# Performance work log

Measured on AMD Instinct MI355X. Metric: run time of the kernel, lower is better.

## Reference

```python
import jax, jax.numpy as jnp
import numpy as np

WINDOW = 7
HEADS = 8
DIM_HEAD = 32
NUM_MEM = 4
EPS = 1e-5


def _rel_pos_indices(window):
    pos = np.arange(window)
    gi, gj = np.meshgrid(pos, pos, indexing='ij')
    grid = np.stack([gi.ravel(), gj.ravel()], axis=-1)          # [w*w, 2]
    rel = grid[:, None, :] - grid[None, :, :] + (window - 1)    # [n, n, 2]
    return jnp.asarray(rel[..., 0] * (2 * window - 1) + rel[..., 1])  # [n, n]


def setup_inputs() -> dict:
    key = jax.random.key(0)
    ks = jax.random.split(key, 5)
    dim = 256
    return {
        'x': jax.random.normal(ks[0], (16, 16, 16, 7, 7, dim), jnp.float32),
        'gamma': jnp.ones((dim,), jnp.float32),
        'w_qkv': jax.random.normal(ks[1], (dim, 3 * dim), jnp.float32) * 0.02,
        'mem_kv': jax.random.normal(ks[2], (2, HEADS, NUM_MEM, DIM_HEAD), jnp.float32),
        'rel_bias_table': jax.random.normal(ks[3], ((2 * WINDOW - 1) ** 2, HEADS), jnp.float32) * 0.02,
        'w_out': jax.random.normal(ks[4], (dim, dim), jnp.float32) * 0.02,
    }


def reference(x, gamma, w_qkv, mem_kv, rel_bias_table, w_out):
    b, H, W, w1, w2, d = x.shape
    n = w1 * w2
    B = b * H * W
    scale = DIM_HEAD ** -0.5

    # LayerNorm (beta fixed at 0)
    mu = x.mean(-1, keepdims=True)
    var = ((x - mu) ** 2).mean(-1, keepdims=True)
    xn = (x - mu) * jax.lax.rsqrt(var + EPS) * gamma

    xw = xn.reshape(B, n, d)
    qkv = xw @ w_qkv                                  # [B, n, 3d]
    q, k, v = jnp.split(qkv, 3, axis=-1)
    to_heads = lambda t: t.reshape(B, n, HEADS, DIM_HEAD).transpose(0, 2, 1, 3)  # bhnd
    q = to_heads(q) * scale
    k = to_heads(k)
    v = to_heads(v)

    # memory kv, broadcast over batch-of-windows
    mk = jnp.broadcast_to(mem_kv[0][None], (B, HEADS, NUM_MEM, DIM_HEAD))
    mv = jnp.broadcast_to(mem_kv[1][None], (B, HEADS, NUM_MEM, DIM_HEAD))
    k = jnp.concatenate([mk, k], axis=2)              # [B, h, num_mem + n, dh]
    v = jnp.concatenate([mv, v], axis=2)

    sim = jnp.einsum('bhid,bhjd->bhij', q, k)         # [B, h, n, num_mem + n]

    idx = _rel_pos_indices(WINDOW)                    # [n, n] int
    bias = rel_bias_table[idx]                        # [n, n, h]
    bias = jnp.pad(bias, ((0, 0), (NUM_MEM, 0), (0, 0)))  # pad keys at front
    sim = sim + bias.transpose(2, 0, 1)[None]         # [1, h, n, num_mem + n]

    attn = jax.nn.softmax(sim, axis=-1)
    out = jnp.einsum('bhij,bhjd->bhid', attn, v)      # [B, h, n, dh]
    out = out.transpose(0, 2, 1, 3).reshape(B, w1, w2, d)
    out = out @ w_out
    return out.reshape(b, H, W, w1, w2, d)
```

## Files before the change

### kernel.cpp

```cpp
#include <hip/hip_runtime.h>
#include <hip/hip_bf16.h>

typedef __attribute__((ext_vector_type(8))) short bf16x8;
typedef __attribute__((ext_vector_type(4))) float f32x4;

#define NWIN   4096
#define NTOK   49
#define DMODEL 256
#define NHEAD  8
#define DHEAD  32
#define NKEY   53
#define LDX    264
#define LDQK   40
#define LDP    72
#define LDVT   72
#define QK_SHORTS 2560
#define VT_SHORTS 2304
#define PERHEAD   7424
#define LDS_SHORTS (PERHEAD * 8)
#define LDS_BYTES  (LDS_SHORTS * 2)

__device__ __forceinline__ short f2bf(float f) {
  unsigned u = __float_as_uint(f);
  unsigned r = (u + 0x7fffu + ((u >> 16) & 1u)) >> 16;
  return (short)r;
}

__device__ __forceinline__ f32x4 mfma16(bf16x8 a, bf16x8 b, f32x4 c) {
  return __builtin_amdgcn_mfma_f32_16x16x32_bf16(a, b, c, 0, 0, 0);
}

__global__ void k_convert(const float* __restrict__ wqkv, const float* __restrict__ wout,
                          short* __restrict__ wqT, short* __restrict__ woT) {
  int idx = blockIdx.x * 256 + threadIdx.x;
  if (idx < 768 * 256) {
    int n = idx >> 8, k = idx & 255;
    wqT[idx] = f2bf(wqkv[k * 768 + n]);
  }
  if (idx < 256 * 256) {
    int n = idx >> 8, k = idx & 255;
    woT[idx] = f2bf(wout[k * 256 + n]);
  }
}

__global__ __launch_bounds__(512, 2) void k_attn(
    const float* __restrict__ x, const float* __restrict__ gamma,
    const short* __restrict__ wqT, const float* __restrict__ memkv,
    const float* __restrict__ btab, short* __restrict__ aout) {
  extern __shared__ short lds[];
  const int tid = threadIdx.x;
  const int wv = tid >> 6;
  const int lane = tid & 63;
  const int lhi = lane >> 4, llo = lane & 15;
  const int win = blockIdx.x;

  {
    int* w = (int*)lds;
    for (int j = tid; j < 64 * LDX / 2; j += 512) w[j] = 0;
  }
  __syncthreads();

  const float* xwin = x + (size_t)win * (NTOK * DMODEL);
  const float4 g4 = ((const float4*)gamma)[lane];
  for (int row = wv; row < NTOK; row += 8) {
    float4 v = ((const float4*)(xwin + row * DMODEL))[lane];
    float s = v.x + v.y + v.z + v.w;
#pragma unroll
    for (int m = 1; m < 64; m <<= 1) s += __shfl_xor(s, m);
    float mu = s * (1.0f / 256.0f);
    float dx = v.x - mu, dy = v.y - mu, dz = v.z - mu, dw = v.w - mu;
    float s2 = dx * dx + dy * dy + dz * dz + dw * dw;
#pragma unroll
    for (int m = 1; m < 64; m <<= 1) s2 += __shfl_xor(s2, m);
    float rs = rsqrtf(s2 * (1.0f / 256.0f) + 1e-5f);
    short4 o;
    o.x = f2bf(dx * rs * g4.x); o.y = f2bf(dy * rs * g4.y);
    o.z = f2bf(dz * rs * g4.z); o.w = f2bf(dw * rs * g4.w);
    *(short4*)&lds[row * LDX + lane * 4] = o;
  }
  __syncthreads();

  const int h = wv;
  f32x4 acc[4][6] = {};
  {
    const int nr = h * 32 + llo;
    const int nrow[6] = {nr, nr + 16, nr + 256, nr + 272, nr + 512, nr + 528};
    for (int ks = 0; ks < 8; ++ks) {
      bf16x8 a[4];
#pragma unroll
      for (int mt = 0; mt < 4; ++mt)
        a[mt] = *(const bf16x8*)&lds[(mt * 16 + llo) * LDX + ks * 32 + lhi * 8];
#pragma unroll
      for (int nt = 0; nt < 6; ++nt) {
        bf16x8 b = *(const bf16x8*)&wqT[nrow[nt] * 256 + ks * 32 + lhi * 8];
#pragma unroll
        for (int mt = 0; mt < 4; ++mt) acc[mt][nt] = mfma16(a[mt], b, acc[mt][nt]);
      }
    }
  }
  __syncthreads();

  short* qh = lds + wv * PERHEAD;
  short* kh = qh + QK_SHORTS;
  short* vth = kh + QK_SHORTS;
  short* Ph = qh;

  {
    int* w = (int*)qh;
    for (int i = lane; i < PERHEAD / 2; i += 64) w[i] = 0;
  }

  const float qscale = 0.17677669529663687f;
#pragma unroll
  for (int mt = 0; mt < 4; ++mt)
#pragma unroll
    for (int r = 0; r < 4; ++r) {
      int row = mt * 16 + lhi * 4 + r;
      if (row < NTOK) {
        qh[row * LDQK + llo]            = f2bf(acc[mt][0][r] * qscale);
        qh[row * LDQK + 16 + llo]       = f2bf(acc[mt][1][r] * qscale);
        kh[(row + 4) * LDQK + llo]      = f2bf(acc[mt][2][r]);
        kh[(row + 4) * LDQK + 16 + llo] = f2bf(acc[mt][3][r]);
        vth[llo * LDVT + row + 4]        = f2bf(acc[mt][4][r]);
        vth[(llo + 16) * LDVT + row + 4] = f2bf(acc[mt][5][r]);
      }
    }
#pragma unroll
  for (int i = 0; i < 2; ++i) {
    int e = lane + i * 64;
    int m = e >> 5, d = e & 31;
    kh[m * LDQK + d]  = f2bf(memkv[(h * 4 + m) * 32 + d]);
    vth[d * LDVT + m] = f2bf(memkv[1024 + (h * 4 + m) * 32 + d]);
  }

  f32x4 sim[4][4] = {};
  {
    bf16x8 qa[4], kb[4];
#pragma unroll
    for (int mt = 0; mt < 4; ++mt)
      qa[mt] = *(const bf16x8*)&qh[(mt * 16 + llo) * LDQK + lhi * 8];
#pragma unroll
    for (int nt = 0; nt < 4; ++nt)
      kb[nt] = *(const bf16x8*)&kh[(nt * 16 + llo) * LDQK + lhi * 8];
#pragma unroll
    for (int nt = 0; nt < 4; ++nt)
#pragma unroll
      for (int mt = 0; mt < 4; ++mt) sim[mt][nt] = mfma16(qa[mt], kb[nt], sim[mt][nt]);
  }

#pragma unroll
  for (int mt = 0; mt < 4; ++mt)
#pragma unroll
    for (int r = 0; r < 4; ++r) {
      const int qt = mt * 16 + lhi * 4 + r;
      const bool qv = qt < NTOK;
      const int qa_ = qt / 7, qb_ = qt % 7;
      float vals[4];
#pragma unroll
      for (int nt = 0; nt < 4; ++nt) {
        int col = nt * 16 + llo;
        float sv = sim[mt][nt][r];
        if (col >= NKEY) sv = -1e30f;
        else if (qv && col >= 4) {
          int t = col - 4;
          int r0 = qa_ - t / 7 + 6, r1 = qb_ - t % 7 + 6;
          sv += btab[(r0 * 13 + r1) * NHEAD + h];
        }
        vals[nt] = sv;
      }
      float mx = fmaxf(fmaxf(vals[0], vals[1]), fmaxf(vals[2], vals[3]));
#pragma unroll
      for (int m = 1; m < 16; m <<= 1) mx = fmaxf(mx, __shfl_xor(mx, m));
      float p[4], sum = 0.f;
#pragma unroll
      for (int nt = 0; nt < 4; ++nt) { p[nt] = __expf(vals[nt] - mx); sum += p[nt]; }
#pragma unroll
      for (int m = 1; m < 16; m <<= 1) sum += __shfl_xor(sum, m);
      float inv = 1.0f / sum;
#pragma unroll
      for (int nt = 0; nt < 4; ++nt)
        Ph[qt * LDP + nt * 16 + llo] = f2bf(p[nt] * inv);
    }

  f32x4 oacc[4][2] = {};
#pragma unroll
  for (int ks = 0; ks < 2; ++ks) {
    bf16x8 pa[4];
#pragma unroll
    for (int mt = 0; mt < 4; ++mt)
      pa[mt] = *(const bf16x8*)&Ph[(mt * 16 + llo) * LDP + ks * 32 + lhi * 8];
#pragma unroll
    for (int nt = 0; nt < 2; ++nt) {
      bf16x8 vb = *(const bf16x8*)&vth[(nt * 16 + llo) * LDVT + ks * 32 + lhi * 8];
#pragma unroll
      for (int mt = 0; mt < 4; ++mt) oacc[mt][nt] = mfma16(pa[mt], vb, oacc[mt][nt]);
    }
  }

  short* ao = aout + (size_t)win * NTOK * DMODEL;
#pragma unroll
  for (int mt = 0; mt < 4; ++mt)
#pragma unroll
    for (int r = 0; r < 4; ++r) {
      int row = mt * 16 + lhi * 4 + r;
      if (row < NTOK) {
#pragma unroll
        for (int nt = 0; nt < 2; ++nt)
          ao[row * DMODEL + h * DHEAD + nt * 16 + llo] = f2bf(oacc[mt][nt][r]);
      }
    }
}

__global__ __launch_bounds__(256, 2) void k_out(
    const short* __restrict__ aout, const short* __restrict__ woT,
    float* __restrict__ out) {
  __shared__ short At[64 * LDX];
  const int tid = threadIdx.x;
  const int wv = tid >> 6, lane = tid & 63;
  const int lhi = lane >> 4, llo = lane & 15;
  const size_t m0 = (size_t)blockIdx.x * 64;
#pragma unroll
  for (int i = 0; i < 8; ++i) {
    int c = tid + i * 256;
    int row = c >> 5, cc = c & 31;
    *(int4*)&At[row * LDX + cc * 8] = *(const int4*)&aout[(m0 + row) * DMODEL + cc * 8];
  }
  __syncthreads();
  f32x4 acc[4][4] = {};
  for (int ks = 0; ks < 8; ++ks) {
    bf16x8 a[4], b[4];
#pragma unroll
    for (int mt = 0; mt < 4; ++mt)
      a[mt] = *(const bf16x8*)&At[(mt * 16 + llo) * LDX + ks * 32 + lhi * 8];
#pragma unroll
    for (int nt = 0; nt < 4; ++nt)
      b[nt] = *(const bf16x8*)&woT[(wv * 64 + nt * 16 + llo) * 256 + ks * 32 + lhi * 8];
#pragma unroll
    for (int nt = 0; nt < 4; ++nt)
#pragma unroll
      for (int mt = 0; mt < 4; ++mt) acc[mt][nt] = mfma16(a[mt], b[nt], acc[mt][nt]);
  }
#pragma unroll
  for (int mt = 0; mt < 4; ++mt)
#pragma unroll
    for (int nt = 0; nt < 4; ++nt)
#pragma unroll
      for (int r = 0; r < 4; ++r)
        out[(m0 + mt * 16 + lhi * 4 + r) * DMODEL + wv * 64 + nt * 16 + llo] = acc[mt][nt][r];
}

extern "C" void kernel_launch(void* const* d_in, const int* in_sizes, int n_in,
                              void* d_out, int out_size, void* d_ws, size_t ws_size,
                              hipStream_t stream) {
  const float* x     = (const float*)d_in[0];
  const float* gamma = (const float*)d_in[1];
  const float* wqkv  = (const float*)d_in[2];
  const float* memkv = (const float*)d_in[3];
  const float* btab  = (const float*)d_in[4];
  const float* wout  = (const float*)d_in[5];
  float* out = (float*)d_out;

  short* wqT  = (short*)d_ws;
  short* woT  = wqT + 768 * 256;
  short* aout = woT + 256 * 256;

  k_convert<<<768, 256, 0, stream>>>(wqkv, wout, wqT, woT);
  k_attn<<<NWIN, 512, LDS_BYTES, stream>>>(x, gamma, wqT, memkv, btab, aout);
  k_out<<<200704 / 64, 256, 0, stream>>>(aout, woT, out);
}
```

Baseline: 858.9 us.

## Split fused LN/QKV/attention kernel into separate QKV and per-head attention kernels

The single large-LDS attention kernel is split in two. k_lnqkv does LayerNorm and the QKV projection, then writes per-head Q, K and transposed V to global memory. k_attn2 runs one wave per (window, head) and computes softmax attention. A prep kernel also precomputes a dense per-head relative-position bias matrix with the padding mask baked in, plus bf16 memory keys, so the softmax loop drops its index arithmetic. The aim is much lower LDS use per block and higher occupancy, at the cost of hundreds of MB of extra global writes and reads for the Q, K and V intermediates.

```diff
diff --git a/kernel.cpp b/kernel.cpp
--- a/kernel.cpp
+++ b/kernel.cpp
@@ -1,24 +1,11 @@
 #include <hip/hip_runtime.h>
-#include <hip/hip_bf16.h>
 
 typedef __attribute__((ext_vector_type(8))) short bf16x8;
 typedef __attribute__((ext_vector_type(4))) float f32x4;
 
-#define NWIN   4096
-#define NTOK   49
-#define DMODEL 256
-#define NHEAD  8
-#define DHEAD  32
-#define NKEY   53
-#define LDX    264
-#define LDQK   40
-#define LDP    72
-#define LDVT   72
-#define QK_SHORTS 2560
-#define VT_SHORTS 2304
-#define PERHEAD   7424
-#define LDS_SHORTS (PERHEAD * 8)
-#define LDS_BYTES  (LDS_SHORTS * 2)
+#define NWIN 4096
+#define NTOK 49
+#define NHEAD 8
 
 __device__ __forceinline__ short f2bf(float f) {
   unsigned u = __float_as_uint(f);
@@ -30,40 +17,45 @@
   return __builtin_amdgcn_mfma_f32_16x16x32_bf16(a, b, c, 0, 0, 0);
 }
 
-__global__ void k_convert(const float* __restrict__ wqkv, const float* __restrict__ wout,
-                          short* __restrict__ wqT, short* __restrict__ woT) {
+__global__ void k_prep(const float* __restrict__ wqkv, const float* __restrict__ wout,
+                       const float* __restrict__ memkv, const float* __restrict__ btab,
+                       short* __restrict__ wqT, short* __restrict__ woT,
+                       short* __restrict__ memB, float* __restrict__ biasF) {
   int idx = blockIdx.x * 256 + threadIdx.x;
-  if (idx < 768 * 256) {
-    int n = idx >> 8, k = idx & 255;
-    wqT[idx] = f2bf(wqkv[k * 768 + n]);
-  }
-  if (idx < 256 * 256) {
-    int n = idx >> 8, k = idx & 255;
-    woT[idx] = f2bf(wout[k * 256 + n]);
-  }
-}
-
-__global__ __launch_bounds__(512, 2) void k_attn(
+  if (idx < 768 * 256) { int n = idx >> 8, k = idx & 255; wqT[idx] = f2bf(wqkv[k * 768 + n]); }
+  if (idx < 256 * 256) { int n = idx >> 8, k = idx & 255; woT[idx] = f2bf(wout[k * 256 + n]); }
+  if (idx < 2048) memB[idx] = f2bf(memkv[idx]);
+  if (idx < 32768) {
+    int h = idx >> 12, qt = (idx >> 6) & 63, col = idx & 63;
+    float b;
+    if (col >= 53) b = -1e30f;
+    else if (col < 4 || qt >= 49) b = 0.f;
+    else {
+      int t = col - 4;
+      int r0 = qt / 7 - t / 7 + 6, r1 = qt % 7 - t % 7 + 6;
+      b = btab[(r0 * 13 + r1) * NHEAD + h];
+    }
+    biasF[idx] = b;
+  }
+}
+
+__global__ __launch_bounds__(512, 4) void k_lnqkv(
     const float* __restrict__ x, const float* __restrict__ gamma,
     const short* __restrict__ wqT, const float* __restrict__ memkv,
-    const float* __restrict__ btab, short* __restrict__ aout) {
-  extern __shared__ short lds[];
+    short* __restrict__ qg, short* __restrict__ kg, short* __restrict__ vtg) {
+  __shared__ short lds[18432];
   const int tid = threadIdx.x;
-  const int wv = tid >> 6;
-  const int lane = tid & 63;
+  const int wv = tid >> 6, lane = tid & 63;
   const int lhi = lane >> 4, llo = lane & 15;
-  const int win = blockIdx.x;
-
-  {
-    int* w = (int*)lds;
-    for (int j = tid; j < 64 * LDX / 2; j += 512) w[j] = 0;
-  }
-  __syncthreads();
-
-  const float* xwin = x + (size_t)win * (NTOK * DMODEL);
+  const int win = blockIdx.x, h = wv;
+
+  for (int j = tid; j < 8448; j += 512) ((int*)lds)[j] = 0;
+  __syncthreads();
+
+  const float* xwin = x + (size_t)win * (NTOK * 256);
   const float4 g4 = ((const float4*)gamma)[lane];
   for (int row = wv; row < NTOK; row += 8) {
-    float4 v = ((const float4*)(xwin + row * DMODEL))[lane];
+    float4 v = ((const float4*)(xwin + row * 256))[lane];
     float s = v.x + v.y + v.z + v.w;
 #pragma unroll
     for (int m = 1; m < 64; m <<= 1) s += __shfl_xor(s, m);
@@ -76,98 +68,128 @@
     short4 o;
     o.x = f2bf(dx * rs * g4.x); o.y = f2bf(dy * rs * g4.y);
     o.z = f2bf(dz * rs * g4.z); o.w = f2bf(dw * rs * g4.w);
-    *(short4*)&lds[row * LDX + lane * 4] = o;
-  }
-  __syncthreads();
-
-  const int h = wv;
-  f32x4 acc[4][6] = {};
+    *(short4*)&lds[row * 264 + lane * 4] = o;
+  }
+  __syncthreads();
+
+  const int nr = h * 32 + llo;
+  f32x4 a1[4][4] = {};
+  for (int ks = 0; ks < 8; ++ks) {
+    bf16x8 a[4];
+#pragma unroll
+    for (int mt = 0; mt < 4; ++mt)
+      a[mt] = *(const bf16x8*)&lds[(mt * 16 + llo) * 264 + ks * 32 + lhi * 8];
+    const int nrow[4] = {nr, nr + 16, nr + 256, nr + 272};
+#pragma unroll
+    for (int nt = 0; nt < 4; ++nt) {
+      bf16x8 b = *(const bf16x8*)&wqT[nrow[nt] * 256 + ks * 32 + lhi * 8];
+#pragma unroll
+      for (int mt = 0; mt < 4; ++mt) a1[mt][nt] = mfma16(a[mt], b, a1[mt][nt]);
+    }
+  }
   {
-    const int nr = h * 32 + llo;
-    const int nrow[6] = {nr, nr + 16, nr + 256, nr + 272, nr + 512, nr + 528};
-    for (int ks = 0; ks < 8; ++ks) {
-      bf16x8 a[4];
-#pragma unroll
-      for (int mt = 0; mt < 4; ++mt)
-        a[mt] = *(const bf16x8*)&lds[(mt * 16 + llo) * LDX + ks * 32 + lhi * 8];
-#pragma unroll
-      for (int nt = 0; nt < 6; ++nt) {
-        bf16x8 b = *(const bf16x8*)&wqT[nrow[nt] * 256 + ks * 32 + lhi * 8];
-#pragma unroll
-        for (int mt = 0; mt < 4; ++mt) acc[mt][nt] = mfma16(a[mt], b, acc[mt][nt]);
+    const float qscale = 0.17677669529663687f;
+    short* qdst = qg + (size_t)(win * 8 + h) * (NTOK * 32);
+    short* kdst = kg + (size_t)(win * 8 + h) * (NTOK * 32);
+#pragma unroll
+    for (int mt = 0; mt < 4; ++mt)
+#pragma unroll
+      for (int r = 0; r < 4; ++r) {
+        int row = mt * 16 + lhi * 4 + r;
+        if (row < NTOK) {
+          qdst[row * 32 + llo]      = f2bf(a1[mt][0][r] * qscale);
+          qdst[row * 32 + llo + 16] = f2bf(a1[mt][1][r] * qscale);
+          kdst[row * 32 + llo]      = f2bf(a1[mt][2][r]);
+          kdst[row * 32 + llo + 16] = f2bf(a1[mt][3][r]);
+        }
       }
-    }
-  }
-  __syncthreads();
-
-  short* qh = lds + wv * PERHEAD;
-  short* kh = qh + QK_SHORTS;
-  short* vth = kh + QK_SHORTS;
-  short* Ph = qh;
-
-  {
-    int* w = (int*)qh;
-    for (int i = lane; i < PERHEAD / 2; i += 64) w[i] = 0;
-  }
-
-  const float qscale = 0.17677669529663687f;
+  }
+  f32x4 a2[4][2] = {};
+  for (int ks = 0; ks < 8; ++ks) {
+    bf16x8 a[4];
+#pragma unroll
+    for (int mt = 0; mt < 4; ++mt)
+      a[mt] = *(const bf16x8*)&lds[(mt * 16 + llo) * 264 + ks * 32 + lhi * 8];
+    const int nrow[2] = {nr + 512, nr + 528};
+#pragma unroll
+    for (int nt = 0; nt < 2; ++nt) {
+      bf16x8 b = *(const bf16x8*)&wqT[nrow[nt] * 256 + ks * 32 + lhi * 8];
+#pragma unroll
+      for (int mt = 0; mt < 4; ++mt) a2[mt][nt] = mfma16(a[mt], b, a2[mt][nt]);
+    }
+  }
+  __syncthreads();
+  for (int j = tid; j < 9216; j += 512) ((int*)lds)[j] = 0;
+  __syncthreads();
+
+  short* vth = lds + wv * 2304;
 #pragma unroll
   for (int mt = 0; mt < 4; ++mt)
 #pragma unroll
     for (int r = 0; r < 4; ++r) {
       int row = mt * 16 + lhi * 4 + r;
       if (row < NTOK) {
-        qh[row * LDQK + llo]            = f2bf(acc[mt][0][r] * qscale);
-        qh[row * LDQK + 16 + llo]       = f2bf(acc[mt][1][r] * qscale);
-        kh[(row + 4) * LDQK + llo]      = f2bf(acc[mt][2][r]);
-        kh[(row + 4) * LDQK + 16 + llo] = f2bf(acc[mt][3][r]);
-        vth[llo * LDVT + row + 4]        = f2bf(acc[mt][4][r]);
-        vth[(llo + 16) * LDVT + row + 4] = f2bf(acc[mt][5][r]);
+        vth[llo * 72 + row + 4]        = f2bf(a2[mt][0][r]);
+        vth[(llo + 16) * 72 + row + 4] = f2bf(a2[mt][1][r]);
       }
     }
 #pragma unroll
   for (int i = 0; i < 2; ++i) {
-    int e = lane + i * 64;
-    int m = e >> 5, d = e & 31;
-    kh[m * LDQK + d]  = f2bf(memkv[(h * 4 + m) * 32 + d]);
-    vth[d * LDVT + m] = f2bf(memkv[1024 + (h * 4 + m) * 32 + d]);
-  }
+    int e = lane + i * 64, m = e >> 5, d = e & 31;
+    vth[d * 72 + m] = f2bf(memkv[1024 + (h * 4 + m) * 32 + d]);
+  }
+#pragma unroll
+  for (int i = 0; i < 4; ++i) {
+    int c = lane + i * 64, row = c >> 3, co = c & 7;
+    bf16x8 t = *(const bf16x8*)&vth[row * 72 + co * 8];
+    *(bf16x8*)&vtg[((size_t)(win * 8 + h) * 32 + row) * 64 + co * 8] = t;
+  }
+}
+
+__global__ __launch_bounds__(256, 4) void k_attn2(
+    const short* __restrict__ qg, const short* __restrict__ kg,
+    const short* __restrict__ vtg, const short* __restrict__ memB,
+    const float* __restrict__ biasF, short* __restrict__ aout) {
+  __shared__ short P[4][64 * 72];
+  const int tid = threadIdx.x;
+  const int wv = tid >> 6, lane = tid & 63;
+  const int lhi = lane >> 4, llo = lane & 15;
+  const int pid = blockIdx.x * 4 + wv;
+  const int win = pid >> 3, h = pid & 7;
+
+  const short* qp = qg + (size_t)pid * (NTOK * 32);
+  const short* kp = kg + (size_t)pid * (NTOK * 32);
+  const short* vp = vtg + (size_t)pid * (32 * 64);
+
+  bf16x8 qa[4], kb[4];
+#pragma unroll
+  for (int mt = 0; mt < 4; ++mt)
+    qa[mt] = *(const bf16x8*)&qp[(mt * 16 + llo) * 32 + lhi * 8];
+  {
+    const short* p = (llo < 4) ? &memB[(h * 4 + llo) * 32] : &kp[(llo - 4) * 32];
+    kb[0] = *(const bf16x8*)&p[lhi * 8];
+  }
+#pragma unroll
+  for (int nt = 1; nt < 4; ++nt)
+    kb[nt] = *(const bf16x8*)&kp[(nt * 16 + llo - 4) * 32 + lhi * 8];
 
   f32x4 sim[4][4] = {};
-  {
-    bf16x8 qa[4], kb[4];
-#pragma unroll
-    for (int mt = 0; mt < 4; ++mt)
-      qa[mt] = *(const bf16x8*)&qh[(mt * 16 + llo) * LDQK + lhi * 8];
-#pragma unroll
-    for (int nt = 0; nt < 4; ++nt)
-      kb[nt] = *(const bf16x8*)&kh[(nt * 16 + llo) * LDQK + lhi * 8];
-#pragma unroll
-    for (int nt = 0; nt < 4; ++nt)
-#pragma unroll
-      for (int mt = 0; mt < 4; ++mt) sim[mt][nt] = mfma16(qa[mt], kb[nt], sim[mt][nt]);
-  }
-
+#pragma unroll
+  for (int nt = 0; nt < 4; ++nt)
+#pragma unroll
+    for (int mt = 0; mt < 4; ++mt) sim[mt][nt] = mfma16(qa[mt], kb[nt], sim[mt][nt]);
+
+  short* Ph = P[wv];
+  const float* bh = biasF + h * 4096;
 #pragma unroll
   for (int mt = 0; mt < 4; ++mt)
 #pragma unroll
     for (int r = 0; r < 4; ++r) {
       const int qt = mt * 16 + lhi * 4 + r;
-      const bool qv = qt < NTOK;
-      const int qa_ = qt / 7, qb_ = qt % 7;
+      const float* br = bh + qt * 64;
       float vals[4];
 #pragma unroll
-      for (int nt = 0; nt < 4; ++nt) {
-        int col = nt * 16 + llo;
-        float sv = sim[mt][nt][r];
-        if (col >= NKEY) sv = -1e30f;
-        else if (qv && col >= 4) {
-          int t = col - 4;
-          int r0 = qa_ - t / 7 + 6, r1 = qb_ - t % 7 + 6;
-          sv += btab[(r0 * 13 + r1) * NHEAD + h];
-        }
-        vals[nt] = sv;
-      }
+      for (int nt = 0; nt < 4; ++nt) vals[nt] = sim[mt][nt][r] + br[nt * 16 + llo];
       float mx = fmaxf(fmaxf(vals[0], vals[1]), fmaxf(vals[2], vals[3]));
 #pragma unroll
       for (int m = 1; m < 16; m <<= 1) mx = fmaxf(mx, __shfl_xor(mx, m));
@@ -179,7 +201,7 @@
       float inv = 1.0f / sum;
 #pragma unroll
       for (int nt = 0; nt < 4; ++nt)
-        Ph[qt * LDP + nt * 16 + llo] = f2bf(p[nt] * inv);
+        Ph[qt * 72 + nt * 16 + llo] = f2bf(p[nt] * inv);
     }
 
   f32x4 oacc[4][2] = {};
@@ -188,16 +210,16 @@
     bf16x8 pa[4];
 #pragma unroll
     for (int mt = 0; mt < 4; ++mt)
-      pa[mt] = *(const bf16x8*)&Ph[(mt * 16 + llo) * LDP + ks * 32 + lhi * 8];
+      pa[mt] = *(const bf16x8*)&Ph[(mt * 16 + llo) * 72 + ks * 32 + lhi * 8];
 #pragma unroll
     for (int nt = 0; nt < 2; ++nt) {
-      bf16x8 vb = *(const bf16x8*)&vth[(nt * 16 + llo) * LDVT + ks * 32 + lhi * 8];
+      bf16x8 vb = *(const bf16x8*)&vp[(nt * 16 + llo) * 64 + ks * 32 + lhi * 8];
 #pragma unroll
       for (int mt = 0; mt < 4; ++mt) oacc[mt][nt] = mfma16(pa[mt], vb, oacc[mt][nt]);
     }
   }
 
-  short* ao = aout + (size_t)win * NTOK * DMODEL;
+  short* ao = aout + (size_t)win * (NTOK * 256);
 #pragma unroll
   for (int mt = 0; mt < 4; ++mt)
 #pragma unroll
@@ -206,24 +228,23 @@
       if (row < NTOK) {
 #pragma unroll
         for (int nt = 0; nt < 2; ++nt)
-          ao[row * DMODEL + h * DHEAD + nt * 16 + llo] = f2bf(oacc[mt][nt][r]);
+          ao[row * 256 + h * 32 + nt * 16 + llo] = f2bf(oacc[mt][nt][r]);
       }
     }
 }
 
-__global__ __launch_bounds__(256, 2) void k_out(
+__global__ __launch_bounds__(256, 4) void k_out(
     const short* __restrict__ aout, const short* __restrict__ woT,
     float* __restrict__ out) {
-  __shared__ short At[64 * LDX];
+  __shared__ short At[64 * 264];
   const int tid = threadIdx.x;
   const int wv = tid >> 6, lane = tid & 63;
   const int lhi = lane >> 4, llo = lane & 15;
   const size_t m0 = (size_t)blockIdx.x * 64;
 #pragma unroll
   for (int i = 0; i < 8; ++i) {
-    int c = tid + i * 256;
-    int row = c >> 5, cc = c & 31;
-    *(int4*)&At[row * LDX + cc * 8] = *(const int4*)&aout[(m0 + row) * DMODEL + cc * 8];
+    int c = tid + i * 256, row = c >> 5, cc = c & 31;
+    *(int4*)&At[row * 264 + cc * 8] = *(const int4*)&aout[(m0 + row) * 256 + cc * 8];
   }
   __syncthreads();
   f32x4 acc[4][4] = {};
@@ -231,7 +252,7 @@
     bf16x8 a[4], b[4];
 #pragma unroll
     for (int mt = 0; mt < 4; ++mt)
-      a[mt] = *(const bf16x8*)&At[(mt * 16 + llo) * LDX + ks * 32 + lhi * 8];
+      a[mt] = *(const bf16x8*)&At[(mt * 16 + llo) * 264 + ks * 32 + lhi * 8];
 #pragma unroll
     for (int nt = 0; nt < 4; ++nt)
       b[nt] = *(const bf16x8*)&woT[(wv * 64 + nt * 16 + llo) * 256 + ks * 32 + lhi * 8];
@@ -246,7 +267,7 @@
     for (int nt = 0; nt < 4; ++nt)
 #pragma unroll
       for (int r = 0; r < 4; ++r)
-        out[(m0 + mt * 16 + lhi * 4 + r) * DMODEL + wv * 64 + nt * 16 + llo] = acc[mt][nt][r];
+        out[(m0 + mt * 16 + lhi * 4 + r) * 256 + wv * 64 + nt * 16 + llo] = acc[mt][nt][r];
 }
 
 extern "C" void kernel_launch(void* const* d_in, const int* in_sizes, int n_in,
@@ -260,11 +281,17 @@
   const float* wout  = (const float*)d_in[5];
   float* out = (float*)d_out;
 
-  short* wqT  = (short*)d_ws;
-  short* woT  = wqT + 768 * 256;
-  short* aout = woT + 256 * 256;
-
-  k_convert<<<768, 256, 0, stream>>>(wqkv, wout, wqT, woT);
-  k_attn<<<NWIN, 512, LDS_BYTES, stream>>>(x, gamma, wqT, memkv, btab, aout);
-  k_out<<<200704 / 64, 256, 0, stream>>>(aout, woT, out);
-}
+  short* wqT   = (short*)d_ws;
+  short* woT   = wqT + 196608;
+  short* memB  = woT + 65536;
+  float* biasF = (float*)(memB + 2048);
+  short* qg    = (short*)(biasF + 32768);
+  short* kg    = qg + 51380224 + 1024;
+  short* vtg   = kg + 51380224 + 1024;
+  short* aout  = vtg + 67108864;
+
+  k_prep<<<768, 256, 0, stream>>>(wqkv, wout, memkv, btab, wqT, woT, memB, biasF);
+  k_lnqkv<<<NWIN, 512, 0, stream>>>(x, gamma, wqT, memkv, qg, kg, vtg);
+  k_attn2<<<8192, 256, 0, stream>>>(qg, kg, vtg, memB, biasF, aout);
+  k_out<<<3136, 256, 0, stream>>>(aout, woT, out);
+}
```

After: 742.9 us. 1.16x faster.
